# Optimization experiments

Hardware: AMD Instinct MI355X
Metric: run time of the kernel (lower is better)

Reference implementation:

```python
import jax, jax.numpy as jnp
import numpy as np

M, N, D, P = 16, 4096, 128, 8192
H = N // D


def setup_inputs() -> dict:
    key = jax.random.key(0)
    ks = jax.random.split(key, 6)
    s = 1.0 / np.sqrt(N)
    return {
        "X": jax.random.normal(ks[0], (M, N), dtype=jnp.float32),
        "W_q": jax.random.normal(ks[1], (N, N), dtype=jnp.float32) * s,
        "W_k": jax.random.normal(ks[2], (N, N), dtype=jnp.float32) * s,
        "W_v": jax.random.normal(ks[3], (N, N), dtype=jnp.float32) * s,
        "cache_K": jax.random.normal(ks[4], (H, P, D), dtype=jnp.float32),
        "cache_V": jax.random.normal(ks[5], (H, P, D), dtype=jnp.float32),
    }


def reference(X, W_q, W_k, W_v, cache_K, cache_V):
    m = X.shape[0]
    h, p, d = cache_K.shape
    # QKV projections: [M, N] @ [N, N] -> [M, H, D] -> [H, M, D]
    q = (X @ W_q).reshape(m, h, d).transpose(1, 0, 2)
    k = (X @ W_k).reshape(m, h, d).transpose(1, 0, 2)
    v = (X @ W_v).reshape(m, h, d).transpose(1, 0, 2)
    # KV-cache concat along the sequence axis -> [H, P+M, D]
    k_all = jnp.concatenate([cache_K, k], axis=1)
    v_all = jnp.concatenate([cache_V, v], axis=1)
    # attention (note: original applies NO 1/sqrt(D) scaling)
    scores = jnp.einsum('hmd,hpd->hmp', q, k_all)  # [H, M, P+M]
    weights = jax.nn.softmax(scores, axis=-1)
    out = jnp.einsum('hmp,hpd->hmd', weights, v_all)  # [H, M, D]
    return out.transpose(1, 0, 2).reshape(m, h * d)
```

## Files before the change

### kernel.cpp

```cpp
#include <hip/hip_runtime.h>

#define HN 32
#define MM 16
#define DD 128
#define NN 4096
#define PP 8192
#define TP 64
#define NCH 16
#define CHUNKLEN (PP / NCH)

__global__ __launch_bounds__(256) void qkv_kernel(
    const float* __restrict__ X, const float* __restrict__ Wq,
    const float* __restrict__ Wk, const float* __restrict__ Wv,
    float* __restrict__ qkv)
{
    __shared__ float Xs[MM][128];
    const int bx  = blockIdx.x;
    const int mat = bx >> 8;
    const int r   = bx & 255;
    const int ct  = r >> 5;
    const int rc  = r & 31;
    const int col0 = ct << 9;
    const int i0   = rc << 7;
    const float* W = (mat == 0) ? Wq : (mat == 1) ? Wk : Wv;
    const int t = threadIdx.x;

    for (int f = t; f < MM*128; f += 256)
        Xs[f >> 7][f & 127] = X[(f >> 7)*NN + i0 + (f & 127)];
    __syncthreads();

    const int c0 = col0 + t, c1 = col0 + 256 + t;
    float a0[MM], a1[MM];
#pragma unroll
    for (int m = 0; m < MM; ++m) { a0[m] = 0.f; a1[m] = 0.f; }

    for (int i8 = 0; i8 < 128; i8 += 8) {
        const float* Wr = W + (size_t)(i0 + i8) * NN;
        float w0[8], w1[8];
#pragma unroll
        for (int rr = 0; rr < 8; ++rr) {
            w0[rr] = Wr[rr*NN + c0];
            w1[rr] = Wr[rr*NN + c1];
        }
#pragma unroll
        for (int m = 0; m < MM; ++m) {
            float4 xa = *reinterpret_cast<const float4*>(&Xs[m][i8]);
            float4 xb = *reinterpret_cast<const float4*>(&Xs[m][i8 + 4]);
            a0[m] += xa.x*w0[0] + xa.y*w0[1] + xa.z*w0[2] + xa.w*w0[3]
                   + xb.x*w0[4] + xb.y*w0[5] + xb.z*w0[6] + xb.w*w0[7];
            a1[m] += xa.x*w1[0] + xa.y*w1[1] + xa.z*w1[2] + xa.w*w1[3]
                   + xb.x*w1[4] + xb.y*w1[5] + xb.z*w1[6] + xb.w*w1[7];
        }
    }
    float* base = qkv + (size_t)mat * HN*MM*DD;
    const int h0 = c0 >> 7, d0 = c0 & 127;
    const int h1 = c1 >> 7, d1 = c1 & 127;
#pragma unroll
    for (int m = 0; m < MM; ++m) {
        atomicAdd(&base[(h0*MM + m)*DD + d0], a0[m]);
        atomicAdd(&base[(h1*MM + m)*DD + d1], a1[m]);
    }
}

__global__ __launch_bounds__(256, 2) void attn_partial3(
    const float* __restrict__ cacheK, const float* __restrict__ cacheV,
    const float* __restrict__ qkv, float* __restrict__ pmu,
    float* __restrict__ ps, float* __restrict__ pacc)
{
    __shared__ float KA[TP][DD + 4];
    __shared__ float KB[TP][DD + 4];
    __shared__ float Wl[TP][20];

    const int chunk = blockIdx.x;
    const int h     = blockIdx.y;
    const int t     = threadIdx.x;
    const int lane  = t & 63;
    const int wv    = t >> 6;
    const int srow0 = t >> 5;
    const int sg    = t & 31;
    const int psi   = lane >> 4;
    const int g     = lane & 15;

    const float* k_ws = qkv + HN*MM*DD;
    const float* v_ws = qkv + 2*HN*MM*DD;
    const float* Kbase = cacheK + ((size_t)h*PP + (size_t)chunk*CHUNKLEN)*DD;
    const float* Vbase = cacheV + ((size_t)h*PP + (size_t)chunk*CHUNKLEN)*DD;
    const float* qb    = qkv + ((size_t)h*MM + 4*wv)*DD;

    const int nfull = CHUNKLEN / TP;
    const int ntile = nfull + (chunk == NCH - 1 ? 1 : 0);

    float mu0 = -3.0e38f, mu1 = -3.0e38f, mu2 = -3.0e38f, mu3 = -3.0e38f;
    float ss0 = 0.f, ss1 = 0.f, ss2 = 0.f, ss3 = 0.f;
    float acc[4][8];
#pragma unroll
    for (int q = 0; q < 4; ++q)
#pragma unroll
        for (int k = 0; k < 8; ++k) acc[q][k] = 0.f;

    float4 stK[8], stV[8];

    auto issueK = [&](int tt2) {
        if (tt2 < nfull) {
            const float* B = Kbase + (size_t)(tt2*TP)*DD;
#pragma unroll
            for (int rr = 0; rr < 8; ++rr)
                stK[rr] = *reinterpret_cast<const float4*>(B + (size_t)(srow0 + 8*rr)*DD + sg*4);
        } else {
#pragma unroll
            for (int rr = 0; rr < 8; ++rr) {
                const int row = srow0 + 8*rr;
                stK[rr] = (row < MM)
                    ? *reinterpret_cast<const float4*>(k_ws + ((size_t)h*MM + row)*DD + sg*4)
                    : make_float4(0.f, 0.f, 0.f, 0.f);
            }
        }
    };
    auto issueV = [&](int tt2) {
        if (tt2 < nfull) {
            const float* B = Vbase + (size_t)(tt2*TP)*DD;
#pragma unroll
            for (int rr = 0; rr < 8; ++rr)
                stV[rr] = *reinterpret_cast<const float4*>(B + (size_t)(srow0 + 8*rr)*DD + sg*4);
        } else {
#pragma unroll
            for (int rr = 0; rr < 8; ++rr) {
                const int row = srow0 + 8*rr;
                stV[rr] = (row < MM)
                    ? *reinterpret_cast<const float4*>(v_ws + ((size_t)h*MM + row)*DD + sg*4)
                    : make_float4(0.f, 0.f, 0.f, 0.f);
            }
        }
    };

    issueK(0);

    for (int tt = 0; tt < ntile; ++tt) {
        const int valid = (tt < nfull) ? TP : MM;

#pragma unroll
        for (int rr = 0; rr < 8; ++rr)
            *reinterpret_cast<float4*>(&KA[srow0 + 8*rr][sg*4]) = stK[rr];

        issueV(tt);

        __syncthreads();

        float s0 = 0.f, s1 = 0.f, s2 = 0.f, s3 = 0.f;
#pragma unroll 4
        for (int dq = 0; dq < 32; ++dq) {
            float4 k = *reinterpret_cast<const float4*>(&KA[lane][dq*4]);
            const float* qp = qb + dq*4;
            float4 q0 = *reinterpret_cast<const float4*>(qp);
            float4 q1 = *reinterpret_cast<const float4*>(qp + DD);
            float4 q2 = *reinterpret_cast<const float4*>(qp + 2*DD);
            float4 q3 = *reinterpret_cast<const float4*>(qp + 3*DD);
            s0 += k.x*q0.x + k.y*q0.y + k.z*q0.z + k.w*q0.w;
            s1 += k.x*q1.x + k.y*q1.y + k.z*q1.z + k.w*q1.w;
            s2 += k.x*q2.x + k.y*q2.y + k.z*q2.z + k.w*q2.w;
            s3 += k.x*q3.x + k.y*q3.y + k.z*q3.z + k.w*q3.w;
        }
        if (lane >= valid) { s0 = s1 = s2 = s3 = -3.0e38f; }

#pragma unroll
        for (int rr = 0; rr < 8; ++rr)
            *reinterpret_cast<float4*>(&KB[srow0 + 8*rr][sg*4]) = stV[rr];

        if (tt + 1 < ntile) issueK(tt + 1);

        float m0 = s0, m1 = s1, m2 = s2, m3 = s3;
#pragma unroll
        for (int off = 1; off < 64; off <<= 1) {
            m0 = fmaxf(m0, __shfl_xor(m0, off));
            m1 = fmaxf(m1, __shfl_xor(m1, off));
            m2 = fmaxf(m2, __shfl_xor(m2, off));
            m3 = fmaxf(m3, __shfl_xor(m3, off));
        }
        const float n0 = fmaxf(mu0, m0), n1 = fmaxf(mu1, m1);
        const float n2 = fmaxf(mu2, m2), n3 = fmaxf(mu3, m3);
        const float r0 = __expf(mu0 - n0), r1 = __expf(mu1 - n1);
        const float r2_ = __expf(mu2 - n2), r3 = __expf(mu3 - n3);
        float w0 = (lane < valid) ? __expf(s0 - n0) : 0.f;
        float w1 = (lane < valid) ? __expf(s1 - n1) : 0.f;
        float w2 = (lane < valid) ? __expf(s2 - n2) : 0.f;
        float w3 = (lane < valid) ? __expf(s3 - n3) : 0.f;
        float t0s = w0, t1s = w1, t2s = w2, t3s = w3;
#pragma unroll
        for (int off = 1; off < 64; off <<= 1) {
            t0s += __shfl_xor(t0s, off);
            t1s += __shfl_xor(t1s, off);
            t2s += __shfl_xor(t2s, off);
            t3s += __shfl_xor(t3s, off);
        }
        ss0 = ss0*r0 + t0s; ss1 = ss1*r1 + t1s;
        ss2 = ss2*r2_ + t2s; ss3 = ss3*r3 + t3s;
        mu0 = n0; mu1 = n1; mu2 = n2; mu3 = n3;
        *reinterpret_cast<float4*>(&Wl[lane][4*wv]) = make_float4(w0, w1, w2, w3);

        __syncthreads();

#pragma unroll
        for (int k = 0; k < 8; ++k) {
            acc[0][k] *= r0; acc[1][k] *= r1; acc[2][k] *= r2_; acc[3][k] *= r3;
        }
#pragma unroll 4
        for (int i = 0; i < 16; ++i) {
            const int p = psi + 4*i;
            float4 wq = *reinterpret_cast<const float4*>(&Wl[p][4*wv]);
            float4 v0 = *reinterpret_cast<const float4*>(&KB[p][g*8]);
            float4 v1 = *reinterpret_cast<const float4*>(&KB[p][g*8 + 4]);
            acc[0][0] += wq.x*v0.x; acc[0][1] += wq.x*v0.y; acc[0][2] += wq.x*v0.z; acc[0][3] += wq.x*v0.w;
            acc[0][4] += wq.x*v1.x; acc[0][5] += wq.x*v1.y; acc[0][6] += wq.x*v1.z; acc[0][7] += wq.x*v1.w;
            acc[1][0] += wq.y*v0.x; acc[1][1] += wq.y*v0.y; acc[1][2] += wq.y*v0.z; acc[1][3] += wq.y*v0.w;
            acc[1][4] += wq.y*v1.x; acc[1][5] += wq.y*v1.y; acc[1][6] += wq.y*v1.z; acc[1][7] += wq.y*v1.w;
            acc[2][0] += wq.z*v0.x; acc[2][1] += wq.z*v0.y; acc[2][2] += wq.z*v0.z; acc[2][3] += wq.z*v0.w;
            acc[2][4] += wq.z*v1.x; acc[2][5] += wq.z*v1.y; acc[2][6] += wq.z*v1.z; acc[2][7] += wq.z*v1.w;
            acc[3][0] += wq.w*v0.x; acc[3][1] += wq.w*v0.y; acc[3][2] += wq.w*v0.z; acc[3][3] += wq.w*v0.w;
            acc[3][4] += wq.w*v1.x; acc[3][5] += wq.w*v1.y; acc[3][6] += wq.w*v1.z; acc[3][7] += wq.w*v1.w;
        }
    }

#pragma unroll
    for (int q = 0; q < 4; ++q)
#pragma unroll
        for (int k = 0; k < 8; ++k) {
            float v = acc[q][k];
            v += __shfl_xor(v, 16);
            v += __shfl_xor(v, 32);
            acc[q][k] = v;
        }
    if (psi == 0) {
        float* pa = pacc + ((size_t)(h*NCH + chunk)*MM + 4*wv)*DD;
#pragma unroll
        for (int q = 0; q < 4; ++q) {
            *reinterpret_cast<float4*>(pa + q*DD + g*8) =
                make_float4(acc[q][0], acc[q][1], acc[q][2], acc[q][3]);
            *reinterpret_cast<float4*>(pa + q*DD + g*8 + 4) =
                make_float4(acc[q][4], acc[q][5], acc[q][6], acc[q][7]);
        }
    }
    if (lane == 0) {
        const int o = (h*NCH + chunk)*MM + 4*wv;
        pmu[o + 0] = mu0; pmu[o + 1] = mu1; pmu[o + 2] = mu2; pmu[o + 3] = mu3;
        ps [o + 0] = ss0; ps [o + 1] = ss1; ps [o + 2] = ss2; ps [o + 3] = ss3;
    }
}

__global__ __launch_bounds__(128) void combine_kernel(
    const float* __restrict__ pmu, const float* __restrict__ ps,
    const float* __restrict__ pacc, float* __restrict__ out)
{
    const int b = blockIdx.x;
    const int h = b >> 4, m = b & 15;
    const int d = threadIdx.x;
    float gm = -3.0e38f;
#pragma unroll
    for (int c = 0; c < NCH; ++c)
        gm = fmaxf(gm, pmu[(h*NCH + c)*MM + m]);
    float stot = 0.f, a = 0.f;
#pragma unroll
    for (int c = 0; c < NCH; ++c) {
        const float f = __expf(pmu[(h*NCH + c)*MM + m] - gm);
        stot += ps[(h*NCH + c)*MM + m] * f;
        a += pacc[((size_t)(h*NCH + c)*MM + m)*DD + d] * f;
    }
    out[m*NN + h*DD + d] = a / stot;
}

extern "C" void kernel_launch(void* const* d_in, const int* in_sizes, int n_in,
                              void* d_out, int out_size, void* d_ws, size_t ws_size,
                              hipStream_t stream) {
    const float* X  = (const float*)d_in[0];
    const float* Wq = (const float*)d_in[1];
    const float* Wk = (const float*)d_in[2];
    const float* Wv = (const float*)d_in[3];
    const float* cK = (const float*)d_in[4];
    const float* cV = (const float*)d_in[5];
    float* out = (float*)d_out;

    float* ws     = (float*)d_ws;
    float* qkv    = ws;
    float* pmu_p  = ws + 3*HN*MM*DD;
    float* ps_p   = pmu_p + HN*NCH*MM;
    float* pacc_p = ps_p + HN*NCH*MM;

    hipMemsetAsync(qkv, 0, (size_t)3*HN*MM*DD*sizeof(float), stream);
    qkv_kernel<<<768, 256, 0, stream>>>(X, Wq, Wk, Wv, qkv);
    attn_partial3<<<dim3(NCH, HN), 256, 0, stream>>>(cK, cV, qkv, pmu_p, ps_p, pacc_p);
    combine_kernel<<<HN*MM, 128, 0, stream>>>(pmu_p, ps_p, pacc_p, out);
}
```

Measured before the change: 174.7 us.

## Rebalance attention split into 24 even chunks, stage Q in LDS, merge K/V buffers

The attention pass now splits each head's 8208 keys (cache plus new tokens) into 24 equal chunks of 342 rows, so the extra 16-token tail no longer lands on one block. More blocks per head gives more parallelism across the GPU. Q is loaded once into shared memory instead of being re-read from global memory in the inner loop. K and V now share one LDS buffer, with extra barriers, so occupancy can rise to 3 blocks per CU. The QKV projection also unrolls over 16 weight rows per step instead of 8. The risks are added synchronization, per-row bounds branches in the loads, and more partial results to combine.

```diff
diff --git a/kernel.cpp b/kernel.cpp
--- a/kernel.cpp
+++ b/kernel.cpp
@@ -6,8 +6,9 @@
 #define NN 4096
 #define PP 8192
 #define TP 64
-#define NCH 16
-#define CHUNKLEN (PP / NCH)
+#define NCH 24
+#define CLEN 342
+#define NTILE ((CLEN + TP - 1) / TP)
 
 __global__ __launch_bounds__(256) void qkv_kernel(
     const float* __restrict__ X, const float* __restrict__ Wq,
@@ -34,22 +35,28 @@
 #pragma unroll
     for (int m = 0; m < MM; ++m) { a0[m] = 0.f; a1[m] = 0.f; }
 
-    for (int i8 = 0; i8 < 128; i8 += 8) {
-        const float* Wr = W + (size_t)(i0 + i8) * NN;
-        float w0[8], w1[8];
-#pragma unroll
-        for (int rr = 0; rr < 8; ++rr) {
-            w0[rr] = Wr[rr*NN + c0];
-            w1[rr] = Wr[rr*NN + c1];
+    for (int i16 = 0; i16 < 128; i16 += 16) {
+        const float* Wr = W + (size_t)(i0 + i16) * NN;
+        float w0[16], w1[16];
+#pragma unroll
+        for (int rr = 0; rr < 16; ++rr) {
+            w0[rr] = Wr[(size_t)rr*NN + c0];
+            w1[rr] = Wr[(size_t)rr*NN + c1];
         }
 #pragma unroll
         for (int m = 0; m < MM; ++m) {
-            float4 xa = *reinterpret_cast<const float4*>(&Xs[m][i8]);
-            float4 xb = *reinterpret_cast<const float4*>(&Xs[m][i8 + 4]);
+            float4 xa = *reinterpret_cast<const float4*>(&Xs[m][i16]);
+            float4 xb = *reinterpret_cast<const float4*>(&Xs[m][i16 + 4]);
+            float4 xc = *reinterpret_cast<const float4*>(&Xs[m][i16 + 8]);
+            float4 xd = *reinterpret_cast<const float4*>(&Xs[m][i16 + 12]);
             a0[m] += xa.x*w0[0] + xa.y*w0[1] + xa.z*w0[2] + xa.w*w0[3]
-                   + xb.x*w0[4] + xb.y*w0[5] + xb.z*w0[6] + xb.w*w0[7];
+                   + xb.x*w0[4] + xb.y*w0[5] + xb.z*w0[6] + xb.w*w0[7]
+                   + xc.x*w0[8] + xc.y*w0[9] + xc.z*w0[10] + xc.w*w0[11]
+                   + xd.x*w0[12] + xd.y*w0[13] + xd.z*w0[14] + xd.w*w0[15];
             a1[m] += xa.x*w1[0] + xa.y*w1[1] + xa.z*w1[2] + xa.w*w1[3]
-                   + xb.x*w1[4] + xb.y*w1[5] + xb.z*w1[6] + xb.w*w1[7];
+                   + xb.x*w1[4] + xb.y*w1[5] + xb.z*w1[6] + xb.w*w1[7]
+                   + xc.x*w1[8] + xc.y*w1[9] + xc.z*w1[10] + xc.w*w1[11]
+                   + xd.x*w1[12] + xd.y*w1[13] + xd.z*w1[14] + xd.w*w1[15];
         }
     }
     float* base = qkv + (size_t)mat * HN*MM*DD;
@@ -62,20 +69,20 @@
     }
 }
 
-__global__ __launch_bounds__(256, 2) void attn_partial3(
+__global__ __launch_bounds__(256, 3) void attn_partial4(
     const float* __restrict__ cacheK, const float* __restrict__ cacheV,
     const float* __restrict__ qkv, float* __restrict__ pmu,
     float* __restrict__ ps, float* __restrict__ pacc)
 {
-    __shared__ float KA[TP][DD + 4];
-    __shared__ float KB[TP][DD + 4];
+    __shared__ float KV[TP][DD + 4];
+    __shared__ float Qs[MM][DD + 4];
     __shared__ float Wl[TP][20];
 
     const int chunk = blockIdx.x;
     const int h     = blockIdx.y;
     const int t     = threadIdx.x;
     const int lane  = t & 63;
-    const int wv    = t >> 6;
+    const int wv    = __builtin_amdgcn_readfirstlane((int)(threadIdx.x >> 6));
     const int srow0 = t >> 5;
     const int sg    = t & 31;
     const int psi   = lane >> 4;
@@ -83,12 +90,13 @@
 
     const float* k_ws = qkv + HN*MM*DD;
     const float* v_ws = qkv + 2*HN*MM*DD;
-    const float* Kbase = cacheK + ((size_t)h*PP + (size_t)chunk*CHUNKLEN)*DD;
-    const float* Vbase = cacheV + ((size_t)h*PP + (size_t)chunk*CHUNKLEN)*DD;
-    const float* qb    = qkv + ((size_t)h*MM + 4*wv)*DD;
-
-    const int nfull = CHUNKLEN / TP;
-    const int ntile = nfull + (chunk == NCH - 1 ? 1 : 0);
+    const int start = chunk * CLEN;
+
+    for (int f = t; f < MM*32; f += 256) {
+        const int row = f >> 5, c4 = f & 31;
+        *reinterpret_cast<float4*>(&Qs[row][c4*4]) =
+            *reinterpret_cast<const float4*>(qkv + ((size_t)h*MM + row)*DD + c4*4);
+    }
 
     float mu0 = -3.0e38f, mu1 = -3.0e38f, mu2 = -3.0e38f, mu3 = -3.0e38f;
     float ss0 = 0.f, ss1 = 0.f, ss2 = 0.f, ss3 = 0.f;
@@ -101,60 +109,57 @@
     float4 stK[8], stV[8];
 
     auto issueK = [&](int tt2) {
-        if (tt2 < nfull) {
-            const float* B = Kbase + (size_t)(tt2*TP)*DD;
-#pragma unroll
-            for (int rr = 0; rr < 8; ++rr)
-                stK[rr] = *reinterpret_cast<const float4*>(B + (size_t)(srow0 + 8*rr)*DD + sg*4);
-        } else {
-#pragma unroll
-            for (int rr = 0; rr < 8; ++rr) {
-                const int row = srow0 + 8*rr;
-                stK[rr] = (row < MM)
-                    ? *reinterpret_cast<const float4*>(k_ws + ((size_t)h*MM + row)*DD + sg*4)
-                    : make_float4(0.f, 0.f, 0.f, 0.f);
-            }
+#pragma unroll
+        for (int rr = 0; rr < 8; ++rr) {
+            const int vr = start + tt2*TP + srow0 + 8*rr;
+            float4 v = make_float4(0.f, 0.f, 0.f, 0.f);
+            if (vr < PP)
+                v = *reinterpret_cast<const float4*>(cacheK + ((size_t)h*PP + vr)*DD + sg*4);
+            else if (vr < PP + MM)
+                v = *reinterpret_cast<const float4*>(k_ws + ((size_t)h*MM + (vr - PP))*DD + sg*4);
+            stK[rr] = v;
         }
     };
     auto issueV = [&](int tt2) {
-        if (tt2 < nfull) {
-            const float* B = Vbase + (size_t)(tt2*TP)*DD;
-#pragma unroll
-            for (int rr = 0; rr < 8; ++rr)
-                stV[rr] = *reinterpret_cast<const float4*>(B + (size_t)(srow0 + 8*rr)*DD + sg*4);
-        } else {
-#pragma unroll
-            for (int rr = 0; rr < 8; ++rr) {
-                const int row = srow0 + 8*rr;
-                stV[rr] = (row < MM)
-                    ? *reinterpret_cast<const float4*>(v_ws + ((size_t)h*MM + row)*DD + sg*4)
-                    : make_float4(0.f, 0.f, 0.f, 0.f);
-            }
+#pragma unroll
+        for (int rr = 0; rr < 8; ++rr) {
+            const int vr = start + tt2*TP + srow0 + 8*rr;
+            float4 v = make_float4(0.f, 0.f, 0.f, 0.f);
+            if (vr < PP)
+                v = *reinterpret_cast<const float4*>(cacheV + ((size_t)h*PP + vr)*DD + sg*4);
+            else if (vr < PP + MM)
+                v = *reinterpret_cast<const float4*>(v_ws + ((size_t)h*MM + (vr - PP))*DD + sg*4);
+            stV[rr] = v;
         }
     };
 
     issueK(0);
 
-    for (int tt = 0; tt < ntile; ++tt) {
-        const int valid = (tt < nfull) ? TP : MM;
-
+    const float* Q0 = &Qs[4*wv + 0][0];
+    const float* Q1 = &Qs[4*wv + 1][0];
+    const float* Q2 = &Qs[4*wv + 2][0];
+    const float* Q3 = &Qs[4*wv + 3][0];
+
+    for (int tt = 0; tt < NTILE; ++tt) {
+        const int valid = min(TP, CLEN - tt*TP);
+
+        __syncthreads();
 #pragma unroll
         for (int rr = 0; rr < 8; ++rr)
-            *reinterpret_cast<float4*>(&KA[srow0 + 8*rr][sg*4]) = stK[rr];
+            *reinterpret_cast<float4*>(&KV[srow0 + 8*rr][sg*4]) = stK[rr];
 
         issueV(tt);
 
         __syncthreads();
 
         float s0 = 0.f, s1 = 0.f, s2 = 0.f, s3 = 0.f;
-#pragma unroll 4
+#pragma unroll 8
         for (int dq = 0; dq < 32; ++dq) {
-            float4 k = *reinterpret_cast<const float4*>(&KA[lane][dq*4]);
-            const float* qp = qb + dq*4;
-            float4 q0 = *reinterpret_cast<const float4*>(qp);
-            float4 q1 = *reinterpret_cast<const float4*>(qp + DD);
-            float4 q2 = *reinterpret_cast<const float4*>(qp + 2*DD);
-            float4 q3 = *reinterpret_cast<const float4*>(qp + 3*DD);
+            float4 k  = *reinterpret_cast<const float4*>(&KV[lane][dq*4]);
+            float4 q0 = *reinterpret_cast<const float4*>(Q0 + dq*4);
+            float4 q1 = *reinterpret_cast<const float4*>(Q1 + dq*4);
+            float4 q2 = *reinterpret_cast<const float4*>(Q2 + dq*4);
+            float4 q3 = *reinterpret_cast<const float4*>(Q3 + dq*4);
             s0 += k.x*q0.x + k.y*q0.y + k.z*q0.z + k.w*q0.w;
             s1 += k.x*q1.x + k.y*q1.y + k.z*q1.z + k.w*q1.w;
             s2 += k.x*q2.x + k.y*q2.y + k.z*q2.z + k.w*q2.w;
@@ -162,11 +167,12 @@
         }
         if (lane >= valid) { s0 = s1 = s2 = s3 = -3.0e38f; }
 
+        __syncthreads();
 #pragma unroll
         for (int rr = 0; rr < 8; ++rr)
-            *reinterpret_cast<float4*>(&KB[srow0 + 8*rr][sg*4]) = stV[rr];
-
-        if (tt + 1 < ntile) issueK(tt + 1);
+            *reinterpret_cast<float4*>(&KV[srow0 + 8*rr][sg*4]) = stV[rr];
+
+        if (tt + 1 < NTILE) issueK(tt + 1);
 
         float m0 = s0, m1 = s1, m2 = s2, m3 = s3;
 #pragma unroll
@@ -207,8 +213,8 @@
         for (int i = 0; i < 16; ++i) {
             const int p = psi + 4*i;
             float4 wq = *reinterpret_cast<const float4*>(&Wl[p][4*wv]);
-            float4 v0 = *reinterpret_cast<const float4*>(&KB[p][g*8]);
-            float4 v1 = *reinterpret_cast<const float4*>(&KB[p][g*8 + 4]);
+            float4 v0 = *reinterpret_cast<const float4*>(&KV[p][g*8]);
+            float4 v1 = *reinterpret_cast<const float4*>(&KV[p][g*8 + 4]);
             acc[0][0] += wq.x*v0.x; acc[0][1] += wq.x*v0.y; acc[0][2] += wq.x*v0.z; acc[0][3] += wq.x*v0.w;
             acc[0][4] += wq.x*v1.x; acc[0][5] += wq.x*v1.y; acc[0][6] += wq.x*v1.z; acc[0][7] += wq.x*v1.w;
             acc[1][0] += wq.y*v0.x; acc[1][1] += wq.y*v0.y; acc[1][2] += wq.y*v0.z; acc[1][3] += wq.y*v0.w;
@@ -286,6 +292,6 @@
 
     hipMemsetAsync(qkv, 0, (size_t)3*HN*MM*DD*sizeof(float), stream);
     qkv_kernel<<<768, 256, 0, stream>>>(X, Wq, Wk, Wv, qkv);
-    attn_partial3<<<dim3(NCH, HN), 256, 0, stream>>>(cK, cV, qkv, pmu_p, ps_p, pacc_p);
+    attn_partial4<<<dim3(NCH, HN), 256, 0, stream>>>(cK, cV, qkv, pmu_p, ps_p, pacc_p);
     combine_kernel<<<HN*MM, 128, 0, stream>>>(pmu_p, ps_p, pacc_p, out);
 }
```

Result: slower. 197.7 us (+13.2%).

## Split attention into more chunks and read V directly from global memory

Applied to the files above, without the earlier changes.

The KV sequence is split into 32 chunks of 256 rows instead of 16, doubling the number of attention blocks. The register-staged K/V prefetch pipeline is dropped: K is loaded straight into one LDS tile, and V is read directly from global memory in the weighted-sum loop. The tail tile clamps row indices instead of zero-filling and relies on masked scores giving zero weights. The QKV projection also reads X from global memory instead of staging it in LDS. The aim is more parallelism and lower LDS use, at the cost of redundant V reads across the four waves, no load/compute overlap, and a larger partial-results workspace.

```diff
diff --git a/kernel.cpp b/kernel.cpp
--- a/kernel.cpp
+++ b/kernel.cpp
@@ -6,15 +6,14 @@
 #define NN 4096
 #define PP 8192
 #define TP 64
-#define NCH 16
-#define CHUNKLEN (PP / NCH)
+#define NCH 32
+#define CROWS 256
 
 __global__ __launch_bounds__(256) void qkv_kernel(
     const float* __restrict__ X, const float* __restrict__ Wq,
     const float* __restrict__ Wk, const float* __restrict__ Wv,
     float* __restrict__ qkv)
 {
-    __shared__ float Xs[MM][128];
     const int bx  = blockIdx.x;
     const int mat = bx >> 8;
     const int r   = bx & 255;
@@ -25,10 +24,6 @@
     const float* W = (mat == 0) ? Wq : (mat == 1) ? Wk : Wv;
     const int t = threadIdx.x;
 
-    for (int f = t; f < MM*128; f += 256)
-        Xs[f >> 7][f & 127] = X[(f >> 7)*NN + i0 + (f & 127)];
-    __syncthreads();
-
     const int c0 = col0 + t, c1 = col0 + 256 + t;
     float a0[MM], a1[MM];
 #pragma unroll
@@ -39,13 +34,14 @@
         float w0[8], w1[8];
 #pragma unroll
         for (int rr = 0; rr < 8; ++rr) {
-            w0[rr] = Wr[rr*NN + c0];
-            w1[rr] = Wr[rr*NN + c1];
-        }
+            w0[rr] = Wr[(size_t)rr*NN + c0];
+            w1[rr] = Wr[(size_t)rr*NN + c1];
+        }
+        const float* Xr = X + i0 + i8;
 #pragma unroll
         for (int m = 0; m < MM; ++m) {
-            float4 xa = *reinterpret_cast<const float4*>(&Xs[m][i8]);
-            float4 xb = *reinterpret_cast<const float4*>(&Xs[m][i8 + 4]);
+            float4 xa = *reinterpret_cast<const float4*>(Xr + (size_t)m*NN);
+            float4 xb = *reinterpret_cast<const float4*>(Xr + (size_t)m*NN + 4);
             a0[m] += xa.x*w0[0] + xa.y*w0[1] + xa.z*w0[2] + xa.w*w0[3]
                    + xb.x*w0[4] + xb.y*w0[5] + xb.z*w0[6] + xb.w*w0[7];
             a1[m] += xa.x*w1[0] + xa.y*w1[1] + xa.z*w1[2] + xa.w*w1[3]
@@ -62,33 +58,32 @@
     }
 }
 
-__global__ __launch_bounds__(256, 2) void attn_partial3(
+__global__ __launch_bounds__(256, 2) void attn_partial6(
     const float* __restrict__ cacheK, const float* __restrict__ cacheV,
     const float* __restrict__ qkv, float* __restrict__ pmu,
     float* __restrict__ ps, float* __restrict__ pacc)
 {
-    __shared__ float KA[TP][DD + 4];
-    __shared__ float KB[TP][DD + 4];
+    __shared__ float Ks[TP][DD + 4];
     __shared__ float Wl[TP][20];
 
     const int chunk = blockIdx.x;
     const int h     = blockIdx.y;
     const int t     = threadIdx.x;
     const int lane  = t & 63;
-    const int wv    = t >> 6;
-    const int srow0 = t >> 5;
+    const int wv    = __builtin_amdgcn_readfirstlane((int)(threadIdx.x >> 6));
+    const int srow  = t >> 5;
     const int sg    = t & 31;
     const int psi   = lane >> 4;
     const int g     = lane & 15;
 
     const float* k_ws = qkv + HN*MM*DD;
     const float* v_ws = qkv + 2*HN*MM*DD;
-    const float* Kbase = cacheK + ((size_t)h*PP + (size_t)chunk*CHUNKLEN)*DD;
-    const float* Vbase = cacheV + ((size_t)h*PP + (size_t)chunk*CHUNKLEN)*DD;
+    const int start = chunk * CROWS;
+    const float* Kbase = cacheK + ((size_t)h*PP + start)*DD;
+    const float* Vbase = cacheV + ((size_t)h*PP + start)*DD;
     const float* qb    = qkv + ((size_t)h*MM + 4*wv)*DD;
 
-    const int nfull = CHUNKLEN / TP;
-    const int ntile = nfull + (chunk == NCH - 1 ? 1 : 0);
+    const int ntile = 4 + (chunk == NCH - 1 ? 1 : 0);
 
     float mu0 = -3.0e38f, mu1 = -3.0e38f, mu2 = -3.0e38f, mu3 = -3.0e38f;
     float ss0 = 0.f, ss1 = 0.f, ss2 = 0.f, ss3 = 0.f;
@@ -98,58 +93,25 @@
 #pragma unroll
         for (int k = 0; k < 8; ++k) acc[q][k] = 0.f;
 
-    float4 stK[8], stV[8];
-
-    auto issueK = [&](int tt2) {
-        if (tt2 < nfull) {
-            const float* B = Kbase + (size_t)(tt2*TP)*DD;
-#pragma unroll
-            for (int rr = 0; rr < 8; ++rr)
-                stK[rr] = *reinterpret_cast<const float4*>(B + (size_t)(srow0 + 8*rr)*DD + sg*4);
-        } else {
-#pragma unroll
-            for (int rr = 0; rr < 8; ++rr) {
-                const int row = srow0 + 8*rr;
-                stK[rr] = (row < MM)
-                    ? *reinterpret_cast<const float4*>(k_ws + ((size_t)h*MM + row)*DD + sg*4)
-                    : make_float4(0.f, 0.f, 0.f, 0.f);
-            }
-        }
-    };
-    auto issueV = [&](int tt2) {
-        if (tt2 < nfull) {
-            const float* B = Vbase + (size_t)(tt2*TP)*DD;
-#pragma unroll
-            for (int rr = 0; rr < 8; ++rr)
-                stV[rr] = *reinterpret_cast<const float4*>(B + (size_t)(srow0 + 8*rr)*DD + sg*4);
-        } else {
-#pragma unroll
-            for (int rr = 0; rr < 8; ++rr) {
-                const int row = srow0 + 8*rr;
-                stV[rr] = (row < MM)
-                    ? *reinterpret_cast<const float4*>(v_ws + ((size_t)h*MM + row)*DD + sg*4)
-                    : make_float4(0.f, 0.f, 0.f, 0.f);
-            }
-        }
-    };
-
-    issueK(0);
-
     for (int tt = 0; tt < ntile; ++tt) {
-        const int valid = (tt < nfull) ? TP : MM;
-
-#pragma unroll
-        for (int rr = 0; rr < 8; ++rr)
-            *reinterpret_cast<float4*>(&KA[srow0 + 8*rr][sg*4]) = stK[rr];
-
-        issueV(tt);
-
+        const bool tail  = (tt == 4);
+        const int  valid = tail ? MM : TP;
+
+        const float* srcK = tail ? k_ws + (size_t)h*MM*DD
+                                 : Kbase + (size_t)tt*TP*DD;
+#pragma unroll
+        for (int rr = 0; rr < 8; ++rr) {
+            const int row  = srow + 8*rr;
+            const int srcr = tail ? min(row, MM - 1) : row;
+            float4 kk = *reinterpret_cast<const float4*>(srcK + (size_t)srcr*DD + sg*4);
+            *reinterpret_cast<float4*>(&Ks[row][sg*4]) = kk;
+        }
         __syncthreads();
 
         float s0 = 0.f, s1 = 0.f, s2 = 0.f, s3 = 0.f;
-#pragma unroll 4
+#pragma unroll 8
         for (int dq = 0; dq < 32; ++dq) {
-            float4 k = *reinterpret_cast<const float4*>(&KA[lane][dq*4]);
+            float4 k  = *reinterpret_cast<const float4*>(&Ks[lane][dq*4]);
             const float* qp = qb + dq*4;
             float4 q0 = *reinterpret_cast<const float4*>(qp);
             float4 q1 = *reinterpret_cast<const float4*>(qp + DD);
@@ -162,12 +124,6 @@
         }
         if (lane >= valid) { s0 = s1 = s2 = s3 = -3.0e38f; }
 
-#pragma unroll
-        for (int rr = 0; rr < 8; ++rr)
-            *reinterpret_cast<float4*>(&KB[srow0 + 8*rr][sg*4]) = stV[rr];
-
-        if (tt + 1 < ntile) issueK(tt + 1);
-
         float m0 = s0, m1 = s1, m2 = s2, m3 = s3;
 #pragma unroll
         for (int off = 1; off < 64; off <<= 1) {
@@ -179,11 +135,11 @@
         const float n0 = fmaxf(mu0, m0), n1 = fmaxf(mu1, m1);
         const float n2 = fmaxf(mu2, m2), n3 = fmaxf(mu3, m3);
         const float r0 = __expf(mu0 - n0), r1 = __expf(mu1 - n1);
-        const float r2_ = __expf(mu2 - n2), r3 = __expf(mu3 - n3);
-        float w0 = (lane < valid) ? __expf(s0 - n0) : 0.f;
-        float w1 = (lane < valid) ? __expf(s1 - n1) : 0.f;
-        float w2 = (lane < valid) ? __expf(s2 - n2) : 0.f;
-        float w3 = (lane < valid) ? __expf(s3 - n3) : 0.f;
+        const float r2 = __expf(mu2 - n2), r3 = __expf(mu3 - n3);
+        const float w0 = __expf(s0 - n0);
+        const float w1 = __expf(s1 - n1);
+        const float w2 = __expf(s2 - n2);
+        const float w3 = __expf(s3 - n3);
         float t0s = w0, t1s = w1, t2s = w2, t3s = w3;
 #pragma unroll
         for (int off = 1; off < 64; off <<= 1) {
@@ -193,7 +149,7 @@
             t3s += __shfl_xor(t3s, off);
         }
         ss0 = ss0*r0 + t0s; ss1 = ss1*r1 + t1s;
-        ss2 = ss2*r2_ + t2s; ss3 = ss3*r3 + t3s;
+        ss2 = ss2*r2 + t2s; ss3 = ss3*r3 + t3s;
         mu0 = n0; mu1 = n1; mu2 = n2; mu3 = n3;
         *reinterpret_cast<float4*>(&Wl[lane][4*wv]) = make_float4(w0, w1, w2, w3);
 
@@ -201,14 +157,18 @@
 
 #pragma unroll
         for (int k = 0; k < 8; ++k) {
-            acc[0][k] *= r0; acc[1][k] *= r1; acc[2][k] *= r2_; acc[3][k] *= r3;
-        }
+            acc[0][k] *= r0; acc[1][k] *= r1; acc[2][k] *= r2; acc[3][k] *= r3;
+        }
+        const float* srcV = tail ? v_ws + (size_t)h*MM*DD
+                                 : Vbase + (size_t)tt*TP*DD;
 #pragma unroll 4
         for (int i = 0; i < 16; ++i) {
-            const int p = psi + 4*i;
+            const int p    = psi + 4*i;
+            const int srcr = tail ? min(p, MM - 1) : p;
+            const float* vp = srcV + (size_t)srcr*DD + g*8;
             float4 wq = *reinterpret_cast<const float4*>(&Wl[p][4*wv]);
-            float4 v0 = *reinterpret_cast<const float4*>(&KB[p][g*8]);
-            float4 v1 = *reinterpret_cast<const float4*>(&KB[p][g*8 + 4]);
+            float4 v0 = *reinterpret_cast<const float4*>(vp);
+            float4 v1 = *reinterpret_cast<const float4*>(vp + 4);
             acc[0][0] += wq.x*v0.x; acc[0][1] += wq.x*v0.y; acc[0][2] += wq.x*v0.z; acc[0][3] += wq.x*v0.w;
             acc[0][4] += wq.x*v1.x; acc[0][5] += wq.x*v1.y; acc[0][6] += wq.x*v1.z; acc[0][7] += wq.x*v1.w;
             acc[1][0] += wq.y*v0.x; acc[1][1] += wq.y*v0.y; acc[1][2] += wq.y*v0.z; acc[1][3] += wq.y*v0.w;
@@ -229,7 +189,7 @@
             v += __shfl_xor(v, 32);
             acc[q][k] = v;
         }
-    if (psi == 0) {
+    if (lane < 16) {
         float* pa = pacc + ((size_t)(h*NCH + chunk)*MM + 4*wv)*DD;
 #pragma unroll
         for (int q = 0; q < 4; ++q) {
@@ -254,11 +214,11 @@
     const int h = b >> 4, m = b & 15;
     const int d = threadIdx.x;
     float gm = -3.0e38f;
-#pragma unroll
+#pragma unroll 8
     for (int c = 0; c < NCH; ++c)
         gm = fmaxf(gm, pmu[(h*NCH + c)*MM + m]);
     float stot = 0.f, a = 0.f;
-#pragma unroll
+#pragma unroll 8
     for (int c = 0; c < NCH; ++c) {
         const float f = __expf(pmu[(h*NCH + c)*MM + m] - gm);
         stot += ps[(h*NCH + c)*MM + m] * f;
@@ -286,6 +246,6 @@
 
     hipMemsetAsync(qkv, 0, (size_t)3*HN*MM*DD*sizeof(float), stream);
     qkv_kernel<<<768, 256, 0, stream>>>(X, Wq, Wk, Wv, qkv);
-    attn_partial3<<<dim3(NCH, HN), 256, 0, stream>>>(cK, cV, qkv, pmu_p, ps_p, pacc_p);
+    attn_partial6<<<dim3(NCH, HN), 256, 0, stream>>>(cK, cV, qkv, pmu_p, ps_p, pacc_p);
     combine_kernel<<<HN*MM, 128, 0, stream>>>(pmu_p, ps_p, pacc_p, out);
 }
```

Measured after the change: 177.6 us. About the same (+1.7%).
